# Kernel tuning notes

Hardware: AMD Instinct MI355X
Metric: run time of the kernel (lower is better)

Reference implementation:

```python
import jax, jax.numpy as jnp
import numpy as np

T, H = 8192, 2048          # num_tokens, hidden_size
NH, NKV, D = 16, 4, 128    # num_heads, num_kv_heads, head_dim
R = 16                     # gate_low_rank_dim
NORM = 16.0                # gate_logit_normalizer
EPS = 1e-6                 # RMSNorm eps


def setup_inputs() -> dict:
    key = jax.random.key(0)
    ks = jax.random.split(key, 8)
    rnd = lambda k, sh, f: jax.random.normal(k, sh, dtype=jnp.float32) * f
    return {
        "hidden_states": rnd(ks[0], (T, H), 1.0),
        "Wqkv": rnd(ks[1], (H, (NH + 2 * NKV) * D), 0.02),
        "bqkv": rnd(ks[2], ((NH + 2 * NKV) * D,), 0.02),
        "gk_w0": rnd(ks[3], (H, R), 0.02),
        "gk_w1": rnd(ks[4], (R, NKV * D), 0.02),
        "gk_b1": rnd(ks[5], (NKV * D,), 0.02),
        "gnorm_w": jnp.ones((D,), jnp.float32),
        "Wo": rnd(ks[6], (NH * D, H), 0.02),
    }


def _gla_scan(q, k, v, g):
    # q,k,v,g: [NH, T, D]. State S: [D, D] per head.
    def step(S, x):
        qt, kt, vt, gt = x
        S = jnp.exp(gt)[:, None] * S + kt[:, None] * vt[None, :]
        return S, qt @ S

    def per_head(qh, kh, vh, gh):
        S0 = jnp.zeros((D, D), qh.dtype)
        _, o = jax.lax.scan(step, S0, (qh, kh, vh, gh))
        return o  # [T, D]

    return jax.vmap(per_head)(q, k, v, g)  # [NH, T, D]


def reference(hidden_states, Wqkv, bqkv, gk_w0, gk_w1, gk_b1, gnorm_w, Wo):
    # qkv projection (with bias), split into q / k / v
    qkv = hidden_states @ Wqkv + bqkv                    # [T, (NH+2*NKV)*D]
    q, k, v = jnp.split(qkv, [NH * D, NH * D + NKV * D], axis=-1)
    # low-rank gate projection (bias0=False, bias1=True)
    gk = (hidden_states @ gk_w0) @ gk_w1 + gk_b1         # [T, NKV*D]

    q = jax.nn.relu(q).reshape(T, NH, D)                 # feature_map = relu
    k = jax.nn.relu(k).reshape(T, NKV, D)
    v = v.reshape(T, NKV, D)
    gk = jax.nn.log_sigmoid(gk).reshape(T, NKV, D) / NORM

    # GQA: repeat_interleave kv heads to NH heads
    rep = NH // NKV
    k = jnp.repeat(k, rep, axis=1)
    v = jnp.repeat(v, rep, axis=1)
    gk = jnp.repeat(gk, rep, axis=1)

    q = q * (D ** -0.5)                                  # fused_chunk_gla default scale

    qh, kh, vh, gh = (t.transpose(1, 0, 2) for t in (q, k, v, gk))  # [NH, T, D]
    o = _gla_scan(qh, kh, vh, gh)                        # [NH, T, D]

    # per-head RMSNorm over head_dim
    o = o * jax.lax.rsqrt(jnp.mean(o * o, axis=-1, keepdims=True) + EPS) * gnorm_w

    o = o.transpose(1, 0, 2).reshape(T, NH * D)          # h n d -> n (h d)
    return o @ Wo                                        # o_proj (no bias)
```

## Files before the change

kernel.cpp:

```cpp
#include <hip/hip_runtime.h>
#include <hip/hip_bf16.h>
#include <cstdint>

typedef unsigned short u16;
typedef unsigned int u32;
typedef float f32x4 __attribute__((ext_vector_type(4)));
typedef short bf16x8 __attribute__((ext_vector_type(8)));

#define T_TOK 8192
#define HID 2048
#define NH 16
#define NKV 4
#define HD 128
#define QKVN 3072
#define CHUNK 64
#define NC 128

__device__ __forceinline__ float bf2f(u16 h){
  u32 u = ((u32)h) << 16;
  return __builtin_bit_cast(float, u);
}
__device__ __forceinline__ u16 f2bf(float f){
  u32 u = __builtin_bit_cast(u32, f);
  u32 r = (u + 0x7fffu + ((u >> 16) & 1u)) >> 16;
  return (u16)r;
}
__device__ __forceinline__ u32 pack2(float a, float b){
  return (u32)f2bf(a) | ((u32)f2bf(b) << 16);
}
__device__ __forceinline__ void gl2lds16(const u16* g, u16* l){
  __builtin_amdgcn_global_load_lds(
      (const __attribute__((address_space(1))) u32*)g,
      (__attribute__((address_space(3))) u32*)l, 16, 0, 0);
}

__global__ __launch_bounds__(256) void cvt_f2b_kernel(
    const float* __restrict__ in, u16* __restrict__ out, int n8)
{
  int i = blockIdx.x*256 + threadIdx.x;
  if (i >= n8) return;
  const float4* p = (const float4*)(in + (size_t)i*8);
  float4 a = p[0], b = p[1];
  uint4 pk;
  pk.x = pack2(a.x, a.y); pk.y = pack2(a.z, a.w);
  pk.z = pack2(b.x, b.y); pk.w = pack2(b.z, b.w);
  *(uint4*)(out + (size_t)i*8) = pk;
}

#define BM 256
#define BN 256
#define BKV2 64
#define ABUF (BM*BKV2)
#define BBUF (BN*BKV2)
#define BUFU (ABUF + BBUF)

__device__ __forceinline__ int swz(int o){ return o ^ (((o >> 7) & 7) << 4); }

__device__ __forceinline__ void stage16(const u16* g, int ldg, u16* l, int o){
  int p = o ^ (((o >> 7) & 7) << 4);
  gl2lds16(g + (size_t)(p >> 7) * ldg + ((p >> 1) & 63), l + (o >> 1));
}

__device__ __forceinline__ void stage_half(const u16* g, int ldg, u16* lregion,
                                           int half, int tid){
  stage16(g, ldg, lregion, (half*1024 + tid)*16);
  stage16(g, ldg, lregion, (half*1024 + 512 + tid)*16);
}

template<typename YT>
__global__ __launch_bounds__(512, 2) void gemm_v2(
    const u16* __restrict__ X, const u16* __restrict__ Wt,
    const float* __restrict__ bias, const float* __restrict__ ebuf,
    const float* __restrict__ rbuf, YT* __restrict__ Y,
    int M, int N, int K, int mode)
{
  __shared__ u16 lds[2 * BUFU];
  const int tid  = threadIdx.x;
  const int lane = tid & 63;
  const int wave = tid >> 6;
  const int wm = wave >> 2;
  const int wn = wave & 3;
  const int ml = lane & 15, quad = lane >> 4;

  const int nwg = gridDim.x;
  const int chunk = nwg >> 3;
  const int lg = (blockIdx.x & 7) * chunk + (blockIdx.x >> 3);
  const int NBt = N >> 8;
  const int bm0 = (lg / NBt) * BM;
  const int bn0 = (lg % NBt) * BN;

  const u16* gA = X  + (size_t)bm0 * K;
  const u16* gB = Wt + (size_t)bn0 * K;

  f32x4 acc[8][4];
  #pragma unroll
  for (int i = 0; i < 8; i++)
    #pragma unroll
    for (int j = 0; j < 4; j++) acc[i][j] = f32x4{0.f, 0.f, 0.f, 0.f};

  const int NT = K >> 6;

  auto ldfrag = [&](const u16* base, int row, int kk)->bf16x8{
    return *(const bf16x8*)((const char*)base + swz(row*128 + kk*64 + quad*16));
  };

  {
    u16* La0 = lds;
    u16* Lb0 = lds + ABUF;
    stage_half(gB, K, Lb0, 0, tid);
    stage_half(gB, K, Lb0, 1, tid);
    stage_half(gA, K, La0, 0, tid);
    stage_half(gA, K, La0, 1, tid);
  }
  asm volatile("s_waitcnt vmcnt(2)" ::: "memory");
  __builtin_amdgcn_s_barrier();

  for (int t = 0; t < NT; ++t){
    u16* La = lds + (t & 1) * BUFU;
    u16* Lb = La + ABUF;
    u16* Na = lds + ((t + 1) & 1) * BUFU;
    u16* Nb = Na + ABUF;
    const u16* ga = gA + (t + 1) * BKV2;
    const u16* gb = gB + (t + 1) * BKV2;
    const bool st = (t + 1 < NT);

    #pragma unroll
    for (int kk = 0; kk < 2; ++kk){
      bf16x8 af[4], bfr[4];
      #pragma unroll
      for (int j = 0; j < 4; ++j) bfr[j] = ldfrag(Lb, wn*64 + j*16 + ml, kk);
      #pragma unroll
      for (int i = 0; i < 4; ++i) af[i] = ldfrag(La, wm*64 + i*16 + ml, kk);
      if (st){
        if (kk == 0) stage_half(gb, K, Nb, 0, tid);
        else         stage_half(ga, K, Na, 0, tid);
      }
      __builtin_amdgcn_sched_barrier(0);
      __builtin_amdgcn_s_barrier();
      asm volatile("s_waitcnt lgkmcnt(0)" ::: "memory");
      __builtin_amdgcn_sched_barrier(0);
      __builtin_amdgcn_s_setprio(1);
      #pragma unroll
      for (int i = 0; i < 4; ++i)
        #pragma unroll
        for (int j = 0; j < 4; ++j)
          acc[i][j] = __builtin_amdgcn_mfma_f32_16x16x32_bf16(af[i], bfr[j], acc[i][j], 0, 0, 0);
      __builtin_amdgcn_s_setprio(0);
      if (kk == 0){
        if (st) asm volatile("s_waitcnt vmcnt(2)" ::: "memory");
        else    asm volatile("s_waitcnt vmcnt(0)" ::: "memory");
      }
      __builtin_amdgcn_s_barrier();

      #pragma unroll
      for (int i = 0; i < 4; ++i) af[i] = ldfrag(La, 128 + wm*64 + i*16 + ml, kk);
      if (st){
        if (kk == 0) stage_half(gb, K, Nb, 1, tid);
        else         stage_half(ga, K, Na, 1, tid);
      }
      __builtin_amdgcn_sched_barrier(0);
      __builtin_amdgcn_s_barrier();
      asm volatile("s_waitcnt lgkmcnt(0)" ::: "memory");
      __builtin_amdgcn_sched_barrier(0);
      __builtin_amdgcn_s_setprio(1);
      #pragma unroll
      for (int i = 0; i < 4; ++i)
        #pragma unroll
        for (int j = 0; j < 4; ++j)
          acc[4+i][j] = __builtin_amdgcn_mfma_f32_16x16x32_bf16(af[i], bfr[j], acc[4+i][j], 0, 0, 0);
      __builtin_amdgcn_s_setprio(0);
      if (kk == 1 && st)
        asm volatile("s_waitcnt vmcnt(2)" ::: "memory");
      __builtin_amdgcn_s_barrier();
    }
  }

  #pragma unroll
  for (int rh = 0; rh < 2; rh++){
    #pragma unroll
    for (int i = 0; i < 4; i++){
      int row = bm0 + rh*128 + wm*64 + i*16 + quad*4;
      #pragma unroll
      for (int j = 0; j < 4; j++){
        int col = bn0 + wn*64 + j*16 + ml;
        float bv = 0.f;
        if (mode == 1) bv = bias[col];
        #pragma unroll
        for (int rr2 = 0; rr2 < 4; rr2++){
          float v = acc[rh*4+i][j][rr2] + bv;
          if (mode == 1){
            int token = row + rr2;
            int cc = token >> 6, tt = token & 63, ii = col & 127;
            if (col < 2048){
              v = fmaxf(v, 0.f) * 0.08838834764831845f;
              v *= ebuf[(((size_t)cc*4 + (col>>9))*64 + tt)*128 + ii];
            } else if (col < 2560){
              v = fmaxf(v, 0.f);
              v *= rbuf[(((size_t)cc*4 + ((col-2048)>>7))*64 + tt)*128 + ii];
            }
          }
          if (sizeof(YT) == 2) Y[(size_t)(row+rr2)*N + col] = (YT)f2bf(v);
          else                 Y[(size_t)(row+rr2)*N + col] = (YT)v;
        }
      }
    }
  }
}

template<typename YT>
__global__ __launch_bounds__(256) void gemm_v4s(
    const u16* __restrict__ X, const u16* __restrict__ Wt,
    const float* __restrict__ bias, const float* __restrict__ ebuf,
    const float* __restrict__ rbuf, YT* __restrict__ Y,
    int M, int N, int K, int mode)
{
  __shared__ u16 lds[3 * 8192];
  const int tid = threadIdx.x;
  const int lane = tid & 63;
  const int wave = tid >> 6;
  const int wm = wave >> 1, wn = wave & 1;

  const int nwg = gridDim.x;
  const int chunk = nwg >> 3;
  const int lg = (blockIdx.x & 7) * chunk + (blockIdx.x >> 3);
  const int NBt = N >> 7;
  const int bm0 = (lg / NBt) * 128;
  const int bn0 = (lg % NBt) * 128;

  f32x4 acc[4][4];
  #pragma unroll
  for (int i=0;i<4;i++)
    #pragma unroll
    for (int j=0;j<4;j++) acc[i][j] = f32x4{0.f,0.f,0.f,0.f};

  const int row0 = tid >> 2, part8 = (tid & 3) * 8;
  const int mrow = lane & 15, q16b = (lane >> 4) << 4;
  const u16* xb = X  + (size_t)bm0 * K;
  const u16* wb = Wt + (size_t)bn0 * K;

  const int NT = K >> 5;

  auto scol = [&](int rr)->int{
    return (((tid & 3) * 16) ^ (((rr >> 1) & 3) << 4)) >> 1;
  };

  #pragma unroll
  for (int tt = 0; tt < 2; ++tt){
    u16* As = lds + tt * 8192;
    u16* Bs = As + 4096;
    int k0 = tt * 32;
    #pragma unroll
    for (int j=0;j<2;j++){
      int rr = j*64 + row0;
      gl2lds16(xb + (size_t)rr*K + k0 + scol(rr), As + rr*32 + part8);
      gl2lds16(wb + (size_t)rr*K + k0 + scol(rr), Bs + rr*32 + part8);
    }
  }
  asm volatile("s_waitcnt vmcnt(4)" ::: "memory");
  __builtin_amdgcn_s_barrier();

  for (int t = 0; t < NT; ++t){
    u16* As = lds + (t % 3) * 8192;
    u16* Bs = As + 4096;
    if (t + 2 < NT){
      u16* Ns = lds + ((t + 2) % 3) * 8192;
      int k0 = (t + 2) * 32;
      #pragma unroll
      for (int j=0;j<2;j++){
        int rr = j*64 + row0;
        gl2lds16(xb + (size_t)rr*K + k0 + scol(rr), Ns + rr*32 + part8);
        gl2lds16(wb + (size_t)rr*K + k0 + scol(rr), Ns + 4096 + rr*32 + part8);
      }
    }
    bf16x8 af[4], bfr[4];
    #pragma unroll
    for (int i=0;i<4;i++){
      int ra = wm*64 + i*16 + mrow;
      int rb = wn*64 + i*16 + mrow;
      af[i]  = *(const bf16x8*)((const char*)As + ra*64 + (q16b ^ (((ra>>1)&3)<<4)));
      bfr[i] = *(const bf16x8*)((const char*)Bs + rb*64 + (q16b ^ (((rb>>1)&3)<<4)));
    }
    #pragma unroll
    for (int i=0;i<4;i++)
      #pragma unroll
      for (int j=0;j<4;j++)
        acc[i][j] = __builtin_amdgcn_mfma_f32_16x16x32_bf16(af[i], bfr[j], acc[i][j], 0, 0, 0);
    if (t + 2 < NT)      asm volatile("s_waitcnt vmcnt(4)" ::: "memory");
    else if (t + 1 < NT) asm volatile("s_waitcnt vmcnt(0)" ::: "memory");
    __builtin_amdgcn_s_barrier();
  }

  #pragma unroll
  for (int i=0;i<4;i++){
    int row = bm0 + wm*64 + i*16 + (lane>>4)*4;
    #pragma unroll
    for (int j=0;j<4;j++){
      int col = bn0 + wn*64 + j*16 + (lane&15);
      float bv = 0.f;
      if (mode == 1) bv = bias[col];
      #pragma unroll
      for (int rr2=0;rr2<4;rr2++){
        float v = acc[i][j][rr2] + bv;
        if (mode == 1){
          int token = row + rr2;
          int cc = token >> 6, tt = token & 63, ii = col & 127;
          if (col < 2048){
            v = fmaxf(v, 0.f) * 0.08838834764831845f;
            v *= ebuf[(((size_t)cc*4 + (col>>9))*64 + tt)*128 + ii];
          } else if (col < 2560){
            v = fmaxf(v, 0.f);
            v *= rbuf[(((size_t)cc*4 + ((col-2048)>>7))*64 + tt)*128 + ii];
          }
        }
        if (sizeof(YT) == 2) Y[(size_t)(row+rr2)*N + col] = (YT)f2bf(v);
        else                 Y[(size_t)(row+rr2)*N + col] = (YT)v;
      }
    }
  }
}

__global__ __launch_bounds__(256) void transpose_f2b(
    const float* __restrict__ in, u16* __restrict__ out, int R, int C)
{
  __shared__ float tile[32][33];
  int c0 = blockIdx.x*32, r0 = blockIdx.y*32;
  int tx = threadIdx.x & 31, ty = threadIdx.x >> 5;
  #pragma unroll
  for (int p=0;p<4;p++) tile[ty + p*8][tx] = in[(size_t)(r0 + ty + p*8)*C + c0 + tx];
  __syncthreads();
  #pragma unroll
  for (int p=0;p<4;p++) out[(size_t)(c0 + ty + p*8)*R + r0 + tx] = f2bf(tile[tx][ty + p*8]);
}

__global__ __launch_bounds__(256) void gk1_kernel(
    const u16* __restrict__ hsb, const float* __restrict__ w0, float* __restrict__ tmp)
{
  int row = blockIdx.x*4 + (threadIdx.x >> 6);
  int lane = threadIdx.x & 63;
  float acc[16];
  #pragma unroll
  for (int n=0;n<16;n++) acc[n]=0.f;
  for (int k = lane; k < HID; k += 64){
    float h = bf2f(hsb[(size_t)row*HID + k]);
    const float* wr = w0 + (size_t)k*16;
    #pragma unroll
    for (int q=0;q<4;q++){
      float4 wv = *(const float4*)(wr + q*4);
      acc[q*4+0] += h*wv.x; acc[q*4+1] += h*wv.y;
      acc[q*4+2] += h*wv.z; acc[q*4+3] += h*wv.w;
    }
  }
  #pragma unroll
  for (int n=0;n<16;n++){
    #pragma unroll
    for (int off=32; off>0; off>>=1)
      acc[n] += __shfl_down(acc[n], off);
  }
  if (lane == 0){
    #pragma unroll
    for (int n=0;n<16;n++) tmp[(size_t)row*16 + n] = acc[n];
  }
}

__global__ __launch_bounds__(256) void gk2_kernel(
    const float* __restrict__ tmp, const float* __restrict__ w1,
    const float* __restrict__ b1, float* __restrict__ g)
{
  int id = blockIdx.x*256 + threadIdx.x;
  int rrow = id >> 9, n = id & 511;
  float a = b1[n];
  #pragma unroll
  for (int k=0;k<16;k++)
    a += tmp[(size_t)rrow*16 + k] * w1[k*512 + n];
  float ls = fminf(a, 0.f) - log1pf(__expf(-fabsf(a)));
  g[id] = ls * 0.0625f;
}

__global__ __launch_bounds__(256) void decay_kernel(
    const float* __restrict__ g, float* __restrict__ ebuf,
    float* __restrict__ rbuf, float* __restrict__ expB)
{
  __shared__ float bL[CHUNK*HD];
  const int c = blockIdx.x, h = blockIdx.y, tid = threadIdx.x;
  for (int off = tid; off < CHUNK*HD; off += 256){
    int t = off >> 7, i = off & 127;
    bL[off] = g[(size_t)(c*CHUNK + t)*512 + h*HD + i];
  }
  __syncthreads();
  if (tid < HD){
    float run = 0.f;
    for (int t=0;t<CHUNK;t++){ run += bL[t*HD + tid]; bL[t*HD + tid] = run; }
    expB[(size_t)(c*NKV + h)*HD + tid] = __expf(run);
  }
  __syncthreads();
  size_t base = (size_t)(c*NKV + h)*CHUNK*HD;
  for (int off = tid; off < CHUNK*HD; off += 256){
    float b = bL[off];
    ebuf[base + off] = __expf(b);
    rbuf[base + off] = __expf(-b);
  }
}

__global__ __launch_bounds__(256) void chunk_stats2_kernel(
    const u16* __restrict__ qkv, const float* __restrict__ expB,
    u16* __restrict__ Kt, u16* __restrict__ Vt)
{
  __shared__ u16 kL[CHUNK*HD];
  __shared__ u16 vL[CHUNK*HD];
  const int c = blockIdx.x, h = blockIdx.y, tid = threadIdx.x;
  #pragma unroll
  for (int it=0; it<4; it++){
    int u = it*256 + tid;
    int t = u >> 4, p = (u & 15)*8;
    size_t tok = (size_t)(c*CHUNK + t);
    *(uint4*)(kL + t*HD + p) = *(const uint4*)(qkv + tok*QKVN + 2048 + h*HD + p);
    *(uint4*)(vL + t*HD + p) = *(const uint4*)(qkv + tok*QKVN + 2560 + h*HD + p);
  }
  __syncthreads();
  {
    int j = tid >> 1, sh = (tid & 1)*32;
    u16* dst = Vt + ((size_t)(c*NKV + h)*HD + j)*CHUNK + sh;
    #pragma unroll
    for (int s2=0; s2<16; s2++){
      u32 a = (u32)vL[(sh + 2*s2)*HD + j] | ((u32)vL[(sh + 2*s2 + 1)*HD + j] << 16);
      *(u32*)(dst + 2*s2) = a;
    }
  }
  int jj = tid >> 1, ih = (tid & 1)*64;
  float acc[64];
  #pragma unroll
  for (int z=0;z<64;z++) acc[z]=0.f;
  for (int t=0;t<CHUNK;t++){
    float vj = bf2f(vL[t*HD + jj]);
    const u32* kp = (const u32*)(kL + t*HD + ih);
    #pragma unroll
    for (int z2=0; z2<32; z2++){
      u32 kw = kp[z2];
      acc[2*z2]   += vj * bf2f((u16)(kw & 0xffffu));
      acc[2*z2+1] += vj * bf2f((u16)(kw >> 16));
    }
  }
  u16* kout = Kt + ((size_t)(c*NKV + h)*HD + jj)*HD + ih;
  const float* eB = expB + (size_t)(c*NKV + h)*HD + ih;
  #pragma unroll
  for (int z2=0; z2<32; z2++)
    *(u32*)(kout + 2*z2) = pack2(acc[2*z2]*eB[2*z2], acc[2*z2+1]*eB[2*z2+1]);
}

__global__ __launch_bounds__(256) void state_scan2_kernel(
    const u16* __restrict__ Kt, const float* __restrict__ expB, u16* __restrict__ St)
{
  int wid = blockIdx.x;
  int h = wid >> 6;
  int j = (wid & 63)*2 + (threadIdx.x >> 7);
  int i = threadIdx.x & 127;
  size_t base = ((size_t)h*HD + j)*HD + i;
  float S = 0.f;
  for (int cc=0; cc<NC; cc++){
    size_t off = (size_t)cc*(NKV*HD*HD) + base;
    St[off] = f2bf(S);
    S = expB[((size_t)cc*NKV + h)*HD + i] * S + bf2f(Kt[off]);
  }
}

__global__ __launch_bounds__(256) void attn_fused_kernel(
    const u16* __restrict__ qkv, const u16* __restrict__ St,
    const u16* __restrict__ Vt, const float* __restrict__ gw,
    u16* __restrict__ obuf)
{
  __shared__ u16 qe[64*136];
  __shared__ u16 kb[64*136];
  __shared__ u16 sb[64*136];
  __shared__ u16 vb[128*72];
  __shared__ u16 pb[64*72];
  const int c = blockIdx.x, qh = blockIdx.y, h = qh >> 2;
  const int tid = threadIdx.x, lane = tid & 63, w = tid >> 6;
  const int ml = lane & 15, quad = lane >> 4, q8 = quad * 8;

  #pragma unroll
  for (int it = 0; it < 4; it++){
    int u = it*256 + tid;
    int t = u >> 4, p = (u & 15) * 8;
    size_t tok = (size_t)(c*CHUNK + t);
    *(uint4*)(qe + t*136 + p) = *(const uint4*)(qkv + tok*QKVN + qh*HD + p);
    *(uint4*)(kb + t*136 + p) = *(const uint4*)(qkv + tok*QKVN + 2048 + h*HD + p);
  }
  __syncthreads();

  bf16x8 aq[4];
  #pragma unroll
  for (int kk=0;kk<4;kk++)
    aq[kk] = *(const bf16x8*)(qe + (w*16 + ml)*136 + kk*32 + q8);
  #pragma unroll
  for (int n=0;n<4;n++){
    f32x4 pa = {0.f,0.f,0.f,0.f};
    #pragma unroll
    for (int kk=0;kk<4;kk++){
      bf16x8 bk = *(const bf16x8*)(kb + (n*16 + ml)*136 + kk*32 + q8);
      pa = __builtin_amdgcn_mfma_f32_16x16x32_bf16(aq[kk], bk, pa, 0, 0, 0);
    }
    #pragma unroll
    for (int r=0;r<4;r++){
      int ti = quad*4 + r;
      float v = (w*16 + ti >= n*16 + ml) ? pa[r] : 0.f;
      pb[(w*16 + ti)*72 + n*16 + ml] = f2bf(v);
    }
  }
  #pragma unroll
  for (int it = 0; it < 4; it++){
    int u = it*256 + tid;
    int j = u >> 3, p = (u & 7) * 8;
    *(uint4*)(vb + j*72 + p) =
        *(const uint4*)(Vt + ((size_t)(c*NKV + h)*HD + j)*CHUNK + p);
    int t2 = u >> 4, p2 = (u & 15) * 8;
    *(uint4*)(sb + t2*136 + p2) =
        *(const uint4*)(St + ((size_t)(c*NKV + h)*HD + t2)*HD + p2);
  }
  __syncthreads();

  f32x4 o[8];
  #pragma unroll
  for (int n=0;n<8;n++) o[n] = f32x4{0.f,0.f,0.f,0.f};
  bf16x8 ap[2];
  #pragma unroll
  for (int ks=0;ks<2;ks++)
    ap[ks] = *(const bf16x8*)(pb + (w*16 + ml)*72 + ks*32 + q8);
  #pragma unroll
  for (int n=0;n<8;n++)
    #pragma unroll
    for (int ks=0;ks<2;ks++){
      bf16x8 bv = *(const bf16x8*)(vb + (n*16 + ml)*72 + ks*32 + q8);
      o[n] = __builtin_amdgcn_mfma_f32_16x16x32_bf16(ap[ks], bv, o[n], 0, 0, 0);
    }
  #pragma unroll
  for (int n=0;n<4;n++)
    #pragma unroll
    for (int kk=0;kk<4;kk++){
      bf16x8 bs = *(const bf16x8*)(sb + (n*16 + ml)*136 + kk*32 + q8);
      o[n] = __builtin_amdgcn_mfma_f32_16x16x32_bf16(aq[kk], bs, o[n], 0, 0, 0);
    }
  #pragma unroll
  for (int it = 0; it < 4; it++){
    int u = it*256 + tid;
    int t2 = u >> 4, p2 = (u & 15) * 8;
    *(uint4*)(kb + t2*136 + p2) =
        *(const uint4*)(St + ((size_t)(c*NKV + h)*HD + 64 + t2)*HD + p2);
  }
  __syncthreads();
  #pragma unroll
  for (int n=0;n<4;n++)
    #pragma unroll
    for (int kk=0;kk<4;kk++){
      bf16x8 bs = *(const bf16x8*)(kb + (n*16 + ml)*136 + kk*32 + q8);
      o[4+n] = __builtin_amdgcn_mfma_f32_16x16x32_bf16(aq[kk], bs, o[4+n], 0, 0, 0);
    }

  float rstd[4];
  #pragma unroll
  for (int r=0;r<4;r++){
    float s = 0.f;
    #pragma unroll
    for (int n=0;n<8;n++) s += o[n][r]*o[n][r];
    #pragma unroll
    for (int off=1; off<16; off<<=1) s += __shfl_xor(s, off);
    rstd[r] = rsqrtf(s*(1.f/128.f) + 1e-6f);
  }
  #pragma unroll
  for (int n=0;n<8;n++){
    float gwv = gw[n*16 + ml];
    #pragma unroll
    for (int r=0;r<4;r++){
      int t = w*16 + quad*4 + r;
      float val = o[n][r] * rstd[r] * gwv;
      obuf[(size_t)(c*CHUNK + t)*(NH*HD) + qh*HD + n*16 + ml] = f2bf(val);
    }
  }
}

extern "C" void kernel_launch(void* const* d_in, const int* in_sizes, int n_in,
                              void* d_out, int out_size, void* d_ws, size_t ws_size,
                              hipStream_t stream)
{
  const float* hs   = (const float*)d_in[0];
  const float* Wqkv = (const float*)d_in[1];
  const float* bqkv = (const float*)d_in[2];
  const float* w0   = (const float*)d_in[3];
  const float* w1   = (const float*)d_in[4];
  const float* b1   = (const float*)d_in[5];
  const float* gw   = (const float*)d_in[6];
  const float* Wo   = (const float*)d_in[7];
  float* out = (float*)d_out;

  char* ws = (char*)d_ws;
  size_t off = 0;
  auto alloc = [&](size_t bytes)->char*{
    char* p = ws + off; off += (bytes + 255) & ~(size_t)255; return p;
  };
  u16*   hsb   = (u16*)  alloc((size_t)T_TOK*HID*2);
  u16*   Wt1   = (u16*)  alloc((size_t)QKVN*HID*2);
  u16*   Wt2   = (u16*)  alloc((size_t)HID*HID*2);
  u16*   qkv   = (u16*)  alloc((size_t)T_TOK*QKVN*2);
  float* gtmp  = (float*)alloc((size_t)T_TOK*16*4);
  float* g     = (float*)alloc((size_t)T_TOK*512*4);
  float* ebuf  = (float*)alloc((size_t)NC*NKV*CHUNK*HD*4);
  float* rbuf  = (float*)alloc((size_t)NC*NKV*CHUNK*HD*4);
  float* expB  = (float*)alloc((size_t)NC*NKV*HD*4);
  u16*   Kt    = (u16*)  alloc((size_t)NC*NKV*HD*HD*2);
  u16*   St    = (u16*)  alloc((size_t)NC*NKV*HD*HD*2);
  u16*   Vt    = (u16*)  alloc((size_t)NC*NKV*HD*CHUNK*2);
  u16*   obuf  = (u16*)  alloc((size_t)T_TOK*NH*HD*2);

  cvt_f2b_kernel<<<dim3(T_TOK*HID/8/256), 256, 0, stream>>>(hs, hsb, T_TOK*HID/8);
  transpose_f2b<<<dim3(QKVN/32, HID/32), 256, 0, stream>>>(Wqkv, Wt1, HID, QKVN);
  transpose_f2b<<<dim3(HID/32,  HID/32), 256, 0, stream>>>(Wo,   Wt2, HID, HID);
  gk1_kernel<<<dim3(T_TOK/4), 256, 0, stream>>>(hsb, w0, gtmp);
  gk2_kernel<<<dim3(T_TOK*512/256), 256, 0, stream>>>(gtmp, w1, b1, g);
  decay_kernel<<<dim3(NC, NKV), 256, 0, stream>>>(g, ebuf, rbuf, expB);
  gemm_v4s<u16><<<dim3((T_TOK/128)*(QKVN/128)), 256, 0, stream>>>(
      hsb, Wt1, bqkv, ebuf, rbuf, qkv, T_TOK, QKVN, HID, 1);
  chunk_stats2_kernel<<<dim3(NC, NKV), 256, 0, stream>>>(qkv, expB, Kt, Vt);
  state_scan2_kernel<<<dim3(256), 256, 0, stream>>>(Kt, expB, St);
  attn_fused_kernel<<<dim3(NC, NH), 256, 0, stream>>>(qkv, St, Vt, gw, obuf);
  gemm_v2<float><<<dim3((T_TOK/BM)*(HID/BN)), 512, 0, stream>>>(
      obuf, Wt2, nullptr, nullptr, nullptr, out, T_TOK, HID, HID, 0);
}
```

Baseline: 556.9 us.

## Split sequential chunk-state scan into segmented two-pass scan; vectorize gk1 loads

The inter-chunk state recurrence, previously one sequential pass over 128 chunks using only 256 blocks, is split into 8 segments. A first pass computes local segment scans in fp32 plus carries, and a second pass folds in the prefix carries and writes the bf16 states. This exposes eight times more parallelism on a latency-bound serial loop, at the cost of extra fp32 traffic through reused scratch buffers (ebuf, g). The gk1 low-rank projection also switches to 16-byte vectorized loads of hidden states.

```diff
diff --git a/kernel.cpp b/kernel.cpp
--- a/kernel.cpp
+++ b/kernel.cpp
@@ -15,6 +15,8 @@
 #define QKVN 3072
 #define CHUNK 64
 #define NC 128
+#define NSEG 8
+#define SEGLEN 16
 
 __device__ __forceinline__ float bf2f(u16 h){
   u32 u = ((u32)h) << 16;
@@ -340,14 +342,21 @@
   float acc[16];
   #pragma unroll
   for (int n=0;n<16;n++) acc[n]=0.f;
-  for (int k = lane; k < HID; k += 64){
-    float h = bf2f(hsb[(size_t)row*HID + k]);
-    const float* wr = w0 + (size_t)k*16;
-    #pragma unroll
-    for (int q=0;q<4;q++){
-      float4 wv = *(const float4*)(wr + q*4);
-      acc[q*4+0] += h*wv.x; acc[q*4+1] += h*wv.y;
-      acc[q*4+2] += h*wv.z; acc[q*4+3] += h*wv.w;
+  #pragma unroll
+  for (int it=0; it<4; ++it){
+    int k = it*512 + lane*8;
+    uint4 pk = *(const uint4*)(hsb + (size_t)row*HID + k);
+    const u16* hv = (const u16*)&pk;
+    #pragma unroll
+    for (int e=0;e<8;e++){
+      float h = bf2f(hv[e]);
+      const float* wr = w0 + (size_t)(k+e)*16;
+      #pragma unroll
+      for (int q=0;q<4;q++){
+        float4 wv = *(const float4*)(wr + q*4);
+        acc[q*4+0] += h*wv.x; acc[q*4+1] += h*wv.y;
+        acc[q*4+2] += h*wv.z; acc[q*4+3] += h*wv.w;
+      }
     }
   }
   #pragma unroll
@@ -447,19 +456,53 @@
     *(u32*)(kout + 2*z2) = pack2(acc[2*z2]*eB[2*z2], acc[2*z2+1]*eB[2*z2+1]);
 }
 
-__global__ __launch_bounds__(256) void state_scan2_kernel(
-    const u16* __restrict__ Kt, const float* __restrict__ expB, u16* __restrict__ St)
-{
-  int wid = blockIdx.x;
-  int h = wid >> 6;
-  int j = (wid & 63)*2 + (threadIdx.x >> 7);
-  int i = threadIdx.x & 127;
-  size_t base = ((size_t)h*HD + j)*HD + i;
+__global__ __launch_bounds__(256) void scan_a_kernel(
+    const u16* __restrict__ Kt, const float* __restrict__ expB,
+    float* __restrict__ StP, float* __restrict__ carry)
+{
+  size_t u = (size_t)blockIdx.x*256 + threadIdx.x;
+  int i = u & 127;
+  int h = (u >> 14) & 3;
+  int s = (int)(u >> 16);
+  size_t base = (u & 65535);
   float S = 0.f;
-  for (int cc=0; cc<NC; cc++){
+  int c0 = s * SEGLEN;
+  #pragma unroll
+  for (int q = 0; q < SEGLEN; ++q){
+    int cc = c0 + q;
     size_t off = (size_t)cc*(NKV*HD*HD) + base;
-    St[off] = f2bf(S);
+    StP[off] = S;
     S = expB[((size_t)cc*NKV + h)*HD + i] * S + bf2f(Kt[off]);
+  }
+  carry[u] = S;
+}
+
+__global__ __launch_bounds__(256) void scan_c_kernel(
+    const float* __restrict__ StP, const float* __restrict__ expB,
+    const float* __restrict__ carry, u16* __restrict__ St)
+{
+  size_t u = (size_t)blockIdx.x*256 + threadIdx.x;
+  int i = u & 127;
+  int h = (u >> 14) & 3;
+  int s = (int)(u >> 16);
+  size_t elem = u & 65535;
+  float Sst = 0.f;
+  for (int sp = 0; sp < s; ++sp){
+    float A = 1.f;
+    int c0 = sp * SEGLEN;
+    #pragma unroll
+    for (int q = 0; q < SEGLEN; ++q)
+      A *= expB[((size_t)(c0+q)*NKV + h)*HD + i];
+    Sst = carry[(size_t)sp*65536 + elem] + A * Sst;
+  }
+  int c0 = s * SEGLEN;
+  float P = 1.f;
+  #pragma unroll
+  for (int q = 0; q < SEGLEN; ++q){
+    int cc = c0 + q;
+    size_t off = (size_t)cc*(NKV*HD*HD) + elem;
+    St[off] = f2bf(StP[off] + P * Sst);
+    P *= expB[((size_t)cc*NKV + h)*HD + i];
   }
 }
 
@@ -609,6 +652,8 @@
   u16*   St    = (u16*)  alloc((size_t)NC*NKV*HD*HD*2);
   u16*   Vt    = (u16*)  alloc((size_t)NC*NKV*HD*CHUNK*2);
   u16*   obuf  = (u16*)  alloc((size_t)T_TOK*NH*HD*2);
+  float* StP   = ebuf;
+  float* carry = g;
 
   cvt_f2b_kernel<<<dim3(T_TOK*HID/8/256), 256, 0, stream>>>(hs, hsb, T_TOK*HID/8);
   transpose_f2b<<<dim3(QKVN/32, HID/32), 256, 0, stream>>>(Wqkv, Wt1, HID, QKVN);
@@ -619,7 +664,8 @@
   gemm_v4s<u16><<<dim3((T_TOK/128)*(QKVN/128)), 256, 0, stream>>>(
       hsb, Wt1, bqkv, ebuf, rbuf, qkv, T_TOK, QKVN, HID, 1);
   chunk_stats2_kernel<<<dim3(NC, NKV), 256, 0, stream>>>(qkv, expB, Kt, Vt);
-  state_scan2_kernel<<<dim3(256), 256, 0, stream>>>(Kt, expB, St);
+  scan_a_kernel<<<dim3(NSEG*NKV*HD*HD/256), 256, 0, stream>>>(Kt, expB, StP, carry);
+  scan_c_kernel<<<dim3(NSEG*NKV*HD*HD/256), 256, 0, stream>>>(StP, expB, carry, St);
   attn_fused_kernel<<<dim3(NC, NH), 256, 0, stream>>>(qkv, St, Vt, gw, obuf);
   gemm_v2<float><<<dim3((T_TOK/BM)*(HID/BN)), 512, 0, stream>>>(
       obuf, Wt2, nullptr, nullptr, nullptr, out, T_TOK, HID, HID, 0);
```

After: 632.6 us. 1.14x slower.
